# Kernel optimization log

Measured on AMD Instinct MI355X. Metric: run time of the kernel, lower is better.

## Reference

```python
import jax, jax.numpy as jnp
import numpy as np

LAYERS, BLOCKS = 10, 3
N_BLK = LAYERS * BLOCKS
RC, SC, K = 128, 128, 2
IN_CH, COND_CH, OUT_CH = 256, 80, 256
DILATIONS = tuple(2 ** (i % LAYERS) for i in range(N_BLK))
INV_SQRT2 = 0.70710678118


def conv1x1(x, w, b):
    # x: [B, I, T], w: [O, I], b: [O] -> [B, O, T]
    return jnp.einsum('oi,bit->bot', w, x) + b[None, :, None]


def causal_conv(x, w, b, dilation):
    # x: [B, C, T], w: [O, I, K]; left-pad by (K-1)*d == torch pad-both + right slice
    pad = (w.shape[2] - 1) * dilation
    y = jax.lax.conv_general_dilated(
        x, w, window_strides=(1,), padding=[(pad, 0)],
        rhs_dilation=(dilation,), dimension_numbers=('NCH', 'OIH', 'NCH'))
    return y + b[None, :, None]


def setup_inputs() -> dict:
    key = jax.random.key(0)
    ks = jax.random.split(key, 20)
    s = 0.05
    B, T = 2, 8000
    inp = {
        'x': jax.random.normal(ks[0], (B, IN_CH, T), jnp.float32),
        'condition': jax.random.normal(ks[1], (B, COND_CH, T), jnp.float32),
        'input_w': jax.random.normal(ks[2], (RC, IN_CH), jnp.float32) * s,
        'input_b': jax.random.normal(ks[3], (RC,), jnp.float32) * s,
        'dil_w': jax.random.normal(ks[4], (N_BLK, RC, RC, K), jnp.float32) * s,
        'dil_b': jax.random.normal(ks[5], (N_BLK, RC), jnp.float32) * s,
        'gate_w': jax.random.normal(ks[6], (N_BLK, RC, RC), jnp.float32) * s,
        'gate_b': jax.random.normal(ks[7], (N_BLK, RC), jnp.float32) * s,
        'cond_w': jax.random.normal(ks[8], (N_BLK, RC, COND_CH), jnp.float32) * s,
        'cond_b': jax.random.normal(ks[9], (N_BLK, RC), jnp.float32) * s,
        'condg_w': jax.random.normal(ks[10], (N_BLK, RC, COND_CH), jnp.float32) * s,
        'condg_b': jax.random.normal(ks[11], (N_BLK, RC), jnp.float32) * s,
        'res_w': jax.random.normal(ks[12], (N_BLK, RC, RC), jnp.float32) * s,
        'res_b': jax.random.normal(ks[13], (N_BLK, RC), jnp.float32) * s,
        'skip_w': jax.random.normal(ks[14], (N_BLK, SC, RC), jnp.float32) * s,
        'skip_b': jax.random.normal(ks[15], (N_BLK, SC), jnp.float32) * s,
        'out1_w': jax.random.normal(ks[16], (SC, SC), jnp.float32) * s,
        'out1_b': jax.random.normal(ks[17], (SC,), jnp.float32) * s,
        'out2_w': jax.random.normal(ks[18], (OUT_CH, SC), jnp.float32) * s,
        'out2_b': jax.random.normal(ks[19], (OUT_CH,), jnp.float32) * s,
    }
    return inp


def reference(x, condition, input_w, input_b, dil_w, dil_b, gate_w, gate_b,
              cond_w, cond_b, condg_w, condg_b, res_w, res_b,
              skip_w, skip_b, out1_w, out1_b, out2_w, out2_b):
    h = conv1x1(x, input_w, input_b)  # [B, RC, T]
    skip = jnp.zeros_like(conv1x1(h, skip_w[0], skip_b[0]) * 0)  # [B, SC, T]
    for i, d in enumerate(DILATIONS):
        a = causal_conv(h, dil_w[i], dil_b[i], d) + conv1x1(condition, cond_w[i], cond_b[i])
        g = conv1x1(h, gate_w[i], gate_b[i]) + conv1x1(condition, condg_w[i], condg_b[i])
        out = jnp.tanh(a) * jax.nn.sigmoid(g)
        h = (h + conv1x1(out, res_w[i], res_b[i])) * INV_SQRT2
        skip = skip + conv1x1(out, skip_w[i], skip_b[i])
    y = jax.nn.relu(conv1x1(skip, out1_w, out1_b))
    return conv1x1(y, out2_w, out2_b)  # [B, 256, T]
```

## Files before the change

kernel.cpp:

```cpp
#include <hip/hip_runtime.h>

#define T_LEN 8000
#define NTPB 125
#define NBLK 250
#define NLAYER 30
#define GUARD 512
#define HROWS (GUARD + T_LEN)
#define SLAB (HROWS * 128)
#define INV_SQRT2 0.70710678118f

typedef short bf16x8 __attribute__((ext_vector_type(8)));
typedef unsigned uint2v __attribute__((ext_vector_type(2)));
typedef unsigned uint4v __attribute__((ext_vector_type(4)));
typedef float f32x4 __attribute__((ext_vector_type(4)));

#define R_HT  0
#define R_OUT 8192
#define R_CND 16384
#define WB0   22528
#define WB1   38912
#define LDS_SHORTS 55296

#define KLINE 4096
#define LS 106496
#define C1 16384
#define C2 32768
#define C3 49152
#define C4 57344
#define C5 73728
#define C6 90112
#define IN_OFF   3194880
#define OUT1_OFF 3227648
#define OUT2_OFF 3244032

__device__ __forceinline__ unsigned short f2bf_u(float f) {
    union { float f; unsigned u; } v; v.f = f;
    unsigned u = v.u + 0x7FFFu + ((v.u >> 16) & 1u);
    return (unsigned short)(u >> 16);
}
__device__ __forceinline__ short f2bf(float f) { return (short)f2bf_u(f); }

__device__ __forceinline__ unsigned cvtpk(float lo, float hi) {
    unsigned r;
    asm("v_cvt_pk_bf16_f32 %0, %1, %2" : "=v"(r) : "v"(lo), "v"(hi));
    return r;
}

__device__ __forceinline__ float gated_act(float av, float gv) {
    float e  = __expf(-2.f * fabsf(av));
    float th = (1.f - e) * __builtin_amdgcn_rcpf(1.f + e);
    th = (av < 0.f) ? -th : th;
    float sg = __builtin_amdgcn_rcpf(1.f + __expf(-gv));
    return th * sg;
}

__device__ __forceinline__ void ldg16_sc1(bf16x8* d, const short* p) {
    asm volatile("global_load_dwordx4 %0, %1, off sc1" : "=v"(*d) : "v"(p));
}
__device__ __forceinline__ void stg8_sc1(short* p, uint2v v) {
    asm volatile("global_store_dwordx2 %0, %1, off sc1" : : "v"(p), "v"(v) : "memory");
}
__device__ __forceinline__ void st_flag(int* p, int v) {
    __hip_atomic_store(p, v, __ATOMIC_RELAXED, __HIP_MEMORY_SCOPE_AGENT);
}
__device__ __forceinline__ void wait_ge(const int* p, int v) {
    while (__hip_atomic_load(p, __ATOMIC_RELAXED, __HIP_MEMORY_SCOPE_AGENT) < v)
        __builtin_amdgcn_s_sleep(1);
}

__device__ __forceinline__ f32x4 mfma_(bf16x8 a, bf16x8 b, f32x4 c) {
    return __builtin_amdgcn_mfma_f32_16x16x32_bf16(a, b, c, 0, 0, 0);
}

__device__ __forceinline__ void gload_lds16(const short* g, short* l) {
    __builtin_amdgcn_global_load_lds(
        (const __attribute__((address_space(1))) unsigned int*)g,
        (__attribute__((address_space(3))) unsigned int*)l, 16, 0, 0);
}
__device__ __forceinline__ void stageW2(const short* src, short* dst, int wv, int lane) {
    gload_lds16(src + wv * 512 + lane * 8, dst + wv * 512);
    gload_lds16(src + (16 + wv) * 512 + lane * 8, dst + (16 + wv) * 512);
}
__device__ __forceinline__ void stageW1(const short* src, short* dst, int wv, int lane) {
    gload_lds16(src + wv * 512 + lane * 8, dst + wv * 512);
}

template<int NP>
__device__ __forceinline__ void pairN(const short* wb, const short* sm, int boff,
                                      int ks0, int lg, int awoff,
                                      f32x4* ac0, f32x4* ac1)
{
#pragma unroll
    for (int p = 0; p < NP; ++p) {
        bf16x8 B = *(const bf16x8*)&sm[boff + ((ks0 + p) * 4 + lg) * 512];
#pragma unroll
        for (int mt = 0; mt < 2; ++mt) {
            bf16x8 a0 = *(const bf16x8*)&wb[p * 8192 + awoff + mt * 512];
            ac0[mt] = mfma_(a0, B, ac0[mt]);
            bf16x8 a1 = *(const bf16x8*)&wb[p * 8192 + 4096 + awoff + mt * 512];
            ac1[mt] = mfma_(a1, B, ac1[mt]);
        }
    }
}
template<int NP>
__device__ __forceinline__ void singleN(const short* wb, const short* sm, int boff,
                                        int ks0, int lg, int awoff, f32x4* ac)
{
#pragma unroll
    for (int p = 0; p < NP; ++p) {
        bf16x8 B = *(const bf16x8*)&sm[boff + ((ks0 + p) * 4 + lg) * 512];
#pragma unroll
        for (int mt = 0; mt < 2; ++mt) {
            bf16x8 a = *(const bf16x8*)&wb[p * 4096 + awoff + mt * 512];
            ac[mt] = mfma_(a, B, ac[mt]);
        }
    }
}

__global__ __launch_bounds__(256) void k_pack(
    const float* __restrict__ dil_w, const float* __restrict__ gate_w,
    const float* __restrict__ cond_w, const float* __restrict__ condg_w,
    const float* __restrict__ res_w, const float* __restrict__ skip_w,
    const float* __restrict__ input_w, const float* __restrict__ out1_w,
    const float* __restrict__ out2_w,
    const float* __restrict__ dil_b, const float* __restrict__ cond_b,
    const float* __restrict__ gate_b, const float* __restrict__ condg_b,
    short* __restrict__ wp, short* __restrict__ hbt, int* __restrict__ flg)
{
    int gid = blockIdx.x * 256 + threadIdx.x;
    if (gid < 512) flg[gid] = 0;
    {
        int g2 = gid - 512;
        if (g2 >= 0 && g2 < 262144) {
            unsigned* hb32 = (unsigned*)hbt;
            int slab = g2 >> 15, off = g2 & 32767;
            hb32[(size_t)slab * (SLAB / 2) + off] = 0u;
        }
    }
    if (gid >= 6400 * 64) return;
    int fid = gid >> 6, lane = gid & 63;
    int lr = lane & 15, lg = lane >> 4;
    float v[8];
    if (fid < 6240) {
        int layer = fid / 208;
        int r = fid - layer * 208;
        int kl = r >> 3, f = r & 7;
        int m = f * 16 + lr;
        size_t mi = (size_t)layer * 128 + m;
        int mat, ks;
        if      (kl < 8)  { mat = (kl & 1) ? 2 : 1; ks = kl >> 1; }
        else if (kl < 14) { mat = (kl & 1) ? 4 : 3; ks = (kl - 8) >> 1; }
        else if (kl < 18) { mat = 0; ks = kl - 14; }
        else              { mat = (kl & 1) ? 6 : 5; ks = (kl - 18) >> 1; }
        int kb = ks * 32 + lg * 8;
#pragma unroll
        for (int e = 0; e < 8; ++e) {
            int k = kb + e;
            float val;
            switch (mat) {
                case 0:  val = dil_w[(mi * 128 + k) * 2];     break;
                case 1:  val = dil_w[(mi * 128 + k) * 2 + 1]; break;
                case 2:  val = gate_w[mi * 128 + k]; break;
                case 3:  val = (k < 80) ? cond_w[mi * 80 + k]
                               : ((k == 80) ? dil_b[mi] + cond_b[mi] : 0.f); break;
                case 4:  val = (k < 80) ? condg_w[mi * 80 + k]
                               : ((k == 80) ? gate_b[mi] + condg_b[mi] : 0.f); break;
                case 5:  val = res_w[mi * 128 + k]; break;
                default: val = skip_w[mi * 128 + k]; break;
            }
            v[e] = val;
        }
    } else if (fid < 6304) {
        int f = fid - 6240; int ks = f >> 3, fr = f & 7;
        int m = fr * 16 + lr; int kb = ks * 32 + lg * 8;
#pragma unroll
        for (int e = 0; e < 8; ++e) v[e] = input_w[(size_t)m * 256 + kb + e];
    } else if (fid < 6336) {
        int f = fid - 6304; int ks = f >> 3, fr = f & 7;
        int m = fr * 16 + lr; int kb = ks * 32 + lg * 8;
#pragma unroll
        for (int e = 0; e < 8; ++e) v[e] = out1_w[(size_t)m * 128 + kb + e];
    } else {
        int f = fid - 6336; int mt = f & 15; int ks = f >> 4;
        int m = mt * 16 + lr; int kb = ks * 32 + lg * 8;
#pragma unroll
        for (int e = 0; e < 8; ++e) v[e] = out2_w[(size_t)m * 128 + kb + e];
    }
    short* dst = wp + (size_t)fid * 512 + lane * 8;
#pragma unroll
    for (int e = 0; e < 8; ++e) dst[e] = f2bf(v[e]);
}

__global__ __launch_bounds__(1024, 4) void k_wavenet(
    const float* __restrict__ x, const float* __restrict__ cond,
    const short* __restrict__ wp, short* __restrict__ hbt,
    const float* __restrict__ ib, const float* __restrict__ rbias,
    const float* __restrict__ sbias, const float* __restrict__ b1,
    const float* __restrict__ b2, float* __restrict__ outp,
    int* __restrict__ rdy, int* __restrict__ dn)
{
    __shared__ __align__(16) short sm[LDS_SHORTS];

    const int tid  = threadIdx.x;
    const int lane = tid & 63;
    const int wv   = __builtin_amdgcn_readfirstlane(tid >> 6);
    const int wm   = wv & 3;
    const int wn   = wv >> 2;
    const int lr   = lane & 15, lg = lane >> 4;
    const int bidx = blockIdx.x;
    const int b    = bidx / NTPB;
    const int ti   = bidx - b * NTPB;
    const int t0   = ti * 64;
    const int tl   = wn * 16 + lr;
    const int tg   = t0 + tl;
    const int tl8  = tl * 8;
    const int lane8 = lane * 8;
    const int awoff = wm * 1024 + lane8;
    const int chA  = wm * 32 + lg * 4;
    const int kbA  = wm * 4 + (lg >> 1);
    const int e0   = (lg & 1) * 4;

    stageW2(wp + IN_OFF, (short*)&sm[WB0], wv, lane);
    stageW2(wp + IN_OFF + 16384, (short*)&sm[WB1], wv, lane);
    {
        const float* xb = x + (size_t)b * 256 * T_LEN + t0 + lane;
#pragma unroll
        for (int it = 0; it < 2; ++it) {
            int kb = wv * 2 + it;
            unsigned pk[4];
#pragma unroll
            for (int e = 0; e < 4; ++e)
                pk[e] = cvtpk(xb[(size_t)(kb * 8 + 2 * e) * T_LEN],
                              xb[(size_t)(kb * 8 + 2 * e + 1) * T_LEN]);
            *(uint4v*)&sm[(kb * 64 + lane) * 8] = *(uint4v*)pk;
        }
        if (wv < 12) {
            const float* cb = cond + (size_t)b * 80 * T_LEN + t0 + lane;
            unsigned pk[4];
#pragma unroll
            for (int e = 0; e < 4; ++e) {
                int c0 = wv * 8 + 2 * e, c1 = c0 + 1;
                float v0 = (c0 < 80) ? cb[(size_t)c0 * T_LEN] : ((c0 == 80) ? 1.f : 0.f);
                float v1 = (c1 < 80) ? cb[(size_t)c1 * T_LEN] : 0.f;
                pk[e] = cvtpk(v0, v1);
            }
            *(uint4v*)&sm[R_CND + (wv * 64 + lane) * 8] = *(uint4v*)pk;
        }
    }
    __syncthreads();

    f32x4 hres[2] = {{0.f,0.f,0.f,0.f},{0.f,0.f,0.f,0.f}};
    {
        f32x4 acc[2] = {{0.f,0.f,0.f,0.f},{0.f,0.f,0.f,0.f}};
        singleN<4>((const short*)&sm[WB0], sm, tl8, 0, lg, awoff, acc);
        singleN<4>((const short*)&sm[WB1], sm, tl8, 4, lg, awoff, acc);
#pragma unroll
        for (int mt = 0; mt < 2; ++mt) {
            int cb0 = chA + mt * 16;
            f32x4 bv = {ib[cb0], ib[cb0 + 1], ib[cb0 + 2], ib[cb0 + 3]};
            hres[mt] = acc[mt] + bv;
        }
    }
    __syncthreads();
    {
        short* hrow = hbt + (size_t)b * SLAB + (size_t)(GUARD + tg) * 128 + chA;
#pragma unroll
        for (int mt = 0; mt < 2; ++mt) {
            uint2v hv = {cvtpk(hres[mt][0], hres[mt][1]), cvtpk(hres[mt][2], hres[mt][3])};
            stg8_sc1(hrow + mt * 16, hv);
            *(uint2v*)&sm[R_HT + ((kbA + mt * 2) * 64 + tl) * 8 + e0] = hv;
        }
    }
    __syncthreads();
    if (tid == 0) st_flag(&rdy[bidx], 1);

    f32x4 skp[2] = {{0.f,0.f,0.f,0.f},{0.f,0.f,0.f,0.f}};

    for (int li = 0; li < NLAYER; ++li) {
        const int d   = 1 << (li % 10);
        const int ksh = (d + 63) >> 6;
        const short* wl  = wp + (size_t)li * LS;
        const short* hcb = hbt + (size_t)((li & 3) * 2 + b) * SLAB;
        short*       hnb = hbt + (size_t)(((li + 1) & 3) * 2 + b) * SLAB;

        stageW2(wl, (short*)&sm[WB0], wv, lane);
        __syncthreads();
        if (lane == 0 && ti >= ksh) wait_ge(&rdy[bidx - ksh], li + 1);
        bf16x8 Bg[4];
        {
            const short* hr = hcb + (size_t)(GUARD + tg - d) * 128 + lg * 8;
#pragma unroll
            for (int ks = 0; ks < 4; ++ks) ldg16_sc1(&Bg[ks], hr + ks * 32);
        }
        stageW2(wl + C1, (short*)&sm[WB1], wv, lane);
        f32x4 aa[2] = {{0.f,0.f,0.f,0.f},{0.f,0.f,0.f,0.f}};
        f32x4 ag[2] = {{0.f,0.f,0.f,0.f},{0.f,0.f,0.f,0.f}};
        pairN<2>((const short*)&sm[WB0], sm, R_HT + tl8, 0, lg, awoff, aa, ag);
        __syncthreads();
        if (tid == 0) st_flag(&dn[bidx], li + 1);
        stageW2(wl + C2, (short*)&sm[WB0], wv, lane);
        pairN<2>((const short*)&sm[WB1], sm, R_HT + tl8, 2, lg, awoff, aa, ag);
        __syncthreads();
        stageW1(wl + C3, (short*)&sm[WB1], wv, lane);
        pairN<2>((const short*)&sm[WB0], sm, R_CND + tl8, 0, lg, awoff, aa, ag);
        __syncthreads();
        stageW2(wl + C4, (short*)&sm[WB0], wv, lane);
        pairN<1>((const short*)&sm[WB1], sm, R_CND + tl8, 2, lg, awoff, aa, ag);
        __syncthreads();
        stageW2(wl + C5, (short*)&sm[WB1], wv, lane);
        {
            const short* wb = (const short*)&sm[WB0];
#pragma unroll
            for (int ks = 0; ks < 4; ++ks) {
#pragma unroll
                for (int mt = 0; mt < 2; ++mt) {
                    bf16x8 a = *(const bf16x8*)&wb[ks * 4096 + awoff + mt * 512];
                    aa[mt] = mfma_(a, Bg[ks], aa[mt]);
                }
            }
        }
#pragma unroll
        for (int mt = 0; mt < 2; ++mt) {
            uint2v ov = {cvtpk(gated_act(aa[mt][0], ag[mt][0]), gated_act(aa[mt][1], ag[mt][1])),
                         cvtpk(gated_act(aa[mt][2], ag[mt][2]), gated_act(aa[mt][3], ag[mt][3]))};
            *(uint2v*)&sm[R_OUT + ((kbA + mt * 2) * 64 + tl) * 8 + e0] = ov;
        }
        __syncthreads();
        stageW2(wl + C6, (short*)&sm[WB0], wv, lane);
        f32x4 ar[2]  = {{0.f,0.f,0.f,0.f},{0.f,0.f,0.f,0.f}};
        f32x4 as2[2] = {{0.f,0.f,0.f,0.f},{0.f,0.f,0.f,0.f}};
        pairN<2>((const short*)&sm[WB1], sm, R_OUT + tl8, 0, lg, awoff, ar, as2);
        __syncthreads();
        pairN<2>((const short*)&sm[WB0], sm, R_OUT + tl8, 2, lg, awoff, ar, as2);

        const float* rbl = rbias + li * 128 + chA;
        const float* sbl = sbias + li * 128 + chA;
#pragma unroll
        for (int mt = 0; mt < 2; ++mt) {
            f32x4 rbv = {rbl[mt*16], rbl[mt*16+1], rbl[mt*16+2], rbl[mt*16+3]};
            f32x4 sbv = {sbl[mt*16], sbl[mt*16+1], sbl[mt*16+2], sbl[mt*16+3]};
            skp[mt]  = skp[mt] + as2[mt] + sbv;
            hres[mt] = (hres[mt] + ar[mt] + rbv) * INV_SQRT2;
        }
        if (li < NLAYER - 1) {
            if (lane == 0 && li >= 3) {
                int d3 = 1 << ((li - 3) % 10);
                int k3 = (d3 + 63) >> 6;
                if (ti + k3 < NTPB) wait_ge(&dn[bidx + k3], li - 2);
            }
            short* hrow = hnb + (size_t)(GUARD + tg) * 128 + chA;
#pragma unroll
            for (int mt = 0; mt < 2; ++mt) {
                uint2v hv = {cvtpk(hres[mt][0], hres[mt][1]), cvtpk(hres[mt][2], hres[mt][3])};
                stg8_sc1(hrow + mt * 16, hv);
                *(uint2v*)&sm[R_HT + ((kbA + mt * 2) * 64 + tl) * 8 + e0] = hv;
            }
        }
        __syncthreads();
        if (tid == 0 && li < NLAYER - 1) st_flag(&rdy[bidx], li + 2);
    }

#pragma unroll
    for (int mt = 0; mt < 2; ++mt) {
        uint2v sv = {cvtpk(skp[mt][0], skp[mt][1]), cvtpk(skp[mt][2], skp[mt][3])};
        *(uint2v*)&sm[R_HT + ((kbA + mt * 2) * 64 + tl) * 8 + e0] = sv;
    }
    stageW2(wp + OUT1_OFF, (short*)&sm[WB0], wv, lane);
    stageW2(wp + OUT2_OFF, (short*)&sm[WB1], wv, lane);
    __syncthreads();
    f32x4 ay[2] = {{0.f,0.f,0.f,0.f},{0.f,0.f,0.f,0.f}};
    singleN<4>((const short*)&sm[WB0], sm, R_HT + tl8, 0, lg, awoff, ay);
#pragma unroll
    for (int mt = 0; mt < 2; ++mt) {
        int cb0 = chA + mt * 16;
        float y0 = fmaxf(ay[mt][0] + b1[cb0],     0.f);
        float y1 = fmaxf(ay[mt][1] + b1[cb0 + 1], 0.f);
        float y2 = fmaxf(ay[mt][2] + b1[cb0 + 2], 0.f);
        float y3 = fmaxf(ay[mt][3] + b1[cb0 + 3], 0.f);
        uint2v yv = {cvtpk(y0, y1), cvtpk(y2, y3)};
        *(uint2v*)&sm[R_OUT + ((kbA + mt * 2) * 64 + tl) * 8 + e0] = yv;
    }
    __syncthreads();
    stageW2(wp + OUT2_OFF + 16384, (short*)&sm[WB0], wv, lane);
    f32x4 ao[4] = {{0.f,0.f,0.f,0.f},{0.f,0.f,0.f,0.f},
                   {0.f,0.f,0.f,0.f},{0.f,0.f,0.f,0.f}};
    {
        const short* wb = (const short*)&sm[WB1];
#pragma unroll
        for (int ksp = 0; ksp < 2; ++ksp) {
            bf16x8 B = *(const bf16x8*)&sm[R_OUT + tl8 + (ksp * 4 + lg) * 512];
#pragma unroll
            for (int mt = 0; mt < 4; ++mt) {
                int fg = 4 * wm + mt;
                bf16x8 A = *(const bf16x8*)&wb[(ksp * 2 + (fg >> 3)) * 4096 + (fg & 7) * 512 + lane8];
                ao[mt] = mfma_(A, B, ao[mt]);
            }
        }
    }
    __syncthreads();
    {
        const short* wb = (const short*)&sm[WB0];
#pragma unroll
        for (int ksp = 0; ksp < 2; ++ksp) {
            bf16x8 B = *(const bf16x8*)&sm[R_OUT + tl8 + ((2 + ksp) * 4 + lg) * 512];
#pragma unroll
            for (int mt = 0; mt < 4; ++mt) {
                int fg = 4 * wm + mt;
                bf16x8 A = *(const bf16x8*)&wb[(ksp * 2 + (fg >> 3)) * 4096 + (fg & 7) * 512 + lane8];
                ao[mt] = mfma_(A, B, ao[mt]);
            }
        }
    }
#pragma unroll
    for (int mt = 0; mt < 4; ++mt) {
        int ch2 = wm * 64 + mt * 16 + lg * 4;
        float* op = outp + ((size_t)(b * 256 + ch2)) * T_LEN + tg;
        op[0]         = ao[mt][0] + b2[ch2];
        op[T_LEN]     = ao[mt][1] + b2[ch2 + 1];
        op[2 * T_LEN] = ao[mt][2] + b2[ch2 + 2];
        op[3 * T_LEN] = ao[mt][3] + b2[ch2 + 3];
    }
}

extern "C" void kernel_launch(void* const* d_in, const int* in_sizes, int n_in,
                              void* d_out, int out_size, void* d_ws, size_t ws_size,
                              hipStream_t stream)
{
    const float* x       = (const float*)d_in[0];
    const float* cond    = (const float*)d_in[1];
    const float* input_w = (const float*)d_in[2];
    const float* input_b = (const float*)d_in[3];
    const float* dil_w   = (const float*)d_in[4];
    const float* dil_b   = (const float*)d_in[5];
    const float* gate_w  = (const float*)d_in[6];
    const float* gate_b  = (const float*)d_in[7];
    const float* cond_w  = (const float*)d_in[8];
    const float* cond_b  = (const float*)d_in[9];
    const float* condg_w = (const float*)d_in[10];
    const float* condg_b = (const float*)d_in[11];
    const float* res_w   = (const float*)d_in[12];
    const float* res_b   = (const float*)d_in[13];
    const float* skip_w  = (const float*)d_in[14];
    const float* skip_b  = (const float*)d_in[15];
    const float* out1_w  = (const float*)d_in[16];
    const float* out1_b  = (const float*)d_in[17];
    const float* out2_w  = (const float*)d_in[18];
    const float* out2_b  = (const float*)d_in[19];
    float* outp = (float*)d_out;

    short* wpk = (short*)d_ws;
    short* hbt = wpk + (size_t)6400 * 512;
    int*   flg = (int*)(hbt + (size_t)8 * SLAB);
    int*   rdy = flg;
    int*   dn  = flg + 256;

    k_pack<<<1600, 256, 0, stream>>>(dil_w, gate_w, cond_w, condg_w, res_w, skip_w,
                                     input_w, out1_w, out2_w,
                                     dil_b, cond_b, gate_b, condg_b, wpk, hbt, flg);

    void* args[] = {(void*)&x, (void*)&cond, (void*)&wpk, (void*)&hbt,
                    (void*)&input_b, (void*)&res_b, (void*)&skip_b,
                    (void*)&out1_b, (void*)&out2_b, (void*)&outp,
                    (void*)&rdy, (void*)&dn};
    hipLaunchCooperativeKernel((void*)k_wavenet, dim3(NBLK), dim3(1024), args, 0, stream);
}
```

Before: 289.5 us.

## Triple-buffer per-layer weight staging with vmcnt waits instead of full barriers

Replaces the two LDS weight buffers with three rotating buffers, so each layer issues up to three chunk loads ahead and waits only with targeted s_waitcnt vmcnt counts plus raw s_barrier rather than __syncthreads. Bias loads are hoisted to the start of the layer, and the neighbour 'done' flag wait is moved earlier, overlapping the final residual/skip MFMA chunk. The epilogue stages all output weights up front and drops one barrier. The intent is to hide global-to-LDS weight latency behind the MFMA work. In exchange it uses more LDS, and correctness now rests on hand-counted vmcnt values matching how stageW1 and stageW2 issue their loads.

```diff
diff --git a/kernel.cpp b/kernel.cpp
--- a/kernel.cpp
+++ b/kernel.cpp
@@ -17,9 +17,8 @@
 #define R_HT  0
 #define R_OUT 8192
 #define R_CND 16384
-#define WB0   22528
-#define WB1   38912
-#define LDS_SHORTS 55296
+#define WBASE 22528
+#define LDS_SHORTS 71680
 
 #define KLINE 4096
 #define LS 106496
@@ -32,6 +31,10 @@
 #define IN_OFF   3194880
 #define OUT1_OFF 3227648
 #define OUT2_OFF 3244032
+
+#define WAITV(N) asm volatile("s_waitcnt vmcnt(" #N ")" ::: "memory")
+#define LGKM0    asm volatile("s_waitcnt lgkmcnt(0)" ::: "memory")
+#define BAR      asm volatile("s_barrier" ::: "memory")
 
 __device__ __forceinline__ unsigned short f2bf_u(float f) {
     union { float f; unsigned u; } v; v.f = f;
@@ -220,8 +223,8 @@
     const int kbA  = wm * 4 + (lg >> 1);
     const int e0   = (lg & 1) * 4;
 
-    stageW2(wp + IN_OFF, (short*)&sm[WB0], wv, lane);
-    stageW2(wp + IN_OFF + 16384, (short*)&sm[WB1], wv, lane);
+    stageW2(wp + IN_OFF, (short*)&sm[WBASE], wv, lane);
+    stageW2(wp + IN_OFF + 16384, (short*)&sm[WBASE + 16384], wv, lane);
     {
         const float* xb = x + (size_t)b * 256 * T_LEN + t0 + lane;
 #pragma unroll
@@ -252,8 +255,8 @@
     f32x4 hres[2] = {{0.f,0.f,0.f,0.f},{0.f,0.f,0.f,0.f}};
     {
         f32x4 acc[2] = {{0.f,0.f,0.f,0.f},{0.f,0.f,0.f,0.f}};
-        singleN<4>((const short*)&sm[WB0], sm, tl8, 0, lg, awoff, acc);
-        singleN<4>((const short*)&sm[WB1], sm, tl8, 4, lg, awoff, acc);
+        singleN<4>((const short*)&sm[WBASE], sm, tl8, 0, lg, awoff, acc);
+        singleN<4>((const short*)&sm[WBASE + 16384], sm, tl8, 4, lg, awoff, acc);
 #pragma unroll
         for (int mt = 0; mt < 2; ++mt) {
             int cb0 = chA + mt * 16;
@@ -271,50 +274,75 @@
             *(uint2v*)&sm[R_HT + ((kbA + mt * 2) * 64 + tl) * 8 + e0] = hv;
         }
     }
+    asm volatile("s_waitcnt vmcnt(0)" ::: "memory");
     __syncthreads();
     if (tid == 0) st_flag(&rdy[bidx], 1);
 
     f32x4 skp[2] = {{0.f,0.f,0.f,0.f},{0.f,0.f,0.f,0.f}};
 
+    int rot = 0;
     for (int li = 0; li < NLAYER; ++li) {
         const int d   = 1 << (li % 10);
         const int ksh = (d + 63) >> 6;
         const short* wl  = wp + (size_t)li * LS;
         const short* hcb = hbt + (size_t)((li & 3) * 2 + b) * SLAB;
         short*       hnb = hbt + (size_t)(((li + 1) & 3) * 2 + b) * SLAB;
-
-        stageW2(wl, (short*)&sm[WB0], wv, lane);
-        __syncthreads();
+        const int rA = rot;
+        const int rB = (rot + 1) % 3;
+        const int rC = (rot + 2) % 3;
+        short* const sA = (short*)&sm[WBASE + rA * 16384];
+        short* const sB = (short*)&sm[WBASE + rB * 16384];
+        short* const sC = (short*)&sm[WBASE + rC * 16384];
+
         if (lane == 0 && ti >= ksh) wait_ge(&rdy[bidx - ksh], li + 1);
+
+        f32x4 rbv[2], sbv[2];
+        {
+            const float* rbl = rbias + li * 128 + chA;
+            const float* sbl = sbias + li * 128 + chA;
+#pragma unroll
+            for (int mt = 0; mt < 2; ++mt) {
+                rbv[mt] = (f32x4){rbl[mt*16], rbl[mt*16+1], rbl[mt*16+2], rbl[mt*16+3]};
+                sbv[mt] = (f32x4){sbl[mt*16], sbl[mt*16+1], sbl[mt*16+2], sbl[mt*16+3]};
+            }
+        }
+
+        stageW2(wl, sA, wv, lane);
         bf16x8 Bg[4];
         {
             const short* hr = hcb + (size_t)(GUARD + tg - d) * 128 + lg * 8;
 #pragma unroll
             for (int ks = 0; ks < 4; ++ks) ldg16_sc1(&Bg[ks], hr + ks * 32);
         }
-        stageW2(wl + C1, (short*)&sm[WB1], wv, lane);
+        stageW2(wl + C1, sB, wv, lane);
+        stageW2(wl + C2, sC, wv, lane);
+
+        WAITV(8); BAR;
         f32x4 aa[2] = {{0.f,0.f,0.f,0.f},{0.f,0.f,0.f,0.f}};
         f32x4 ag[2] = {{0.f,0.f,0.f,0.f},{0.f,0.f,0.f,0.f}};
-        pairN<2>((const short*)&sm[WB0], sm, R_HT + tl8, 0, lg, awoff, aa, ag);
-        __syncthreads();
+        pairN<2>(sA, sm, R_HT + tl8, 0, lg, awoff, aa, ag);
+
+        WAITV(2); BAR;
         if (tid == 0) st_flag(&dn[bidx], li + 1);
-        stageW2(wl + C2, (short*)&sm[WB0], wv, lane);
-        pairN<2>((const short*)&sm[WB1], sm, R_HT + tl8, 2, lg, awoff, aa, ag);
-        __syncthreads();
-        stageW1(wl + C3, (short*)&sm[WB1], wv, lane);
-        pairN<2>((const short*)&sm[WB0], sm, R_CND + tl8, 0, lg, awoff, aa, ag);
-        __syncthreads();
-        stageW2(wl + C4, (short*)&sm[WB0], wv, lane);
-        pairN<1>((const short*)&sm[WB1], sm, R_CND + tl8, 2, lg, awoff, aa, ag);
-        __syncthreads();
-        stageW2(wl + C5, (short*)&sm[WB1], wv, lane);
+        stageW1(wl + C3, sA, wv, lane);
+        pairN<2>(sB, sm, R_HT + tl8, 2, lg, awoff, aa, ag);
+
+        WAITV(1); BAR;
+        stageW2(wl + C4, sB, wv, lane);
+        pairN<2>(sC, sm, R_CND + tl8, 0, lg, awoff, aa, ag);
+
+        WAITV(2); BAR;
+        stageW2(wl + C5, sC, wv, lane);
+        pairN<1>(sA, sm, R_CND + tl8, 2, lg, awoff, aa, ag);
+
+        WAITV(2); BAR;
+        stageW2(wl + C6, sA, wv, lane);
         {
-            const short* wb = (const short*)&sm[WB0];
 #pragma unroll
             for (int ks = 0; ks < 4; ++ks) {
 #pragma unroll
                 for (int mt = 0; mt < 2; ++mt) {
-                    bf16x8 a = *(const bf16x8*)&wb[ks * 4096 + awoff + mt * 512];
+                    bf16x8 a = *(const bf16x8*)&sB[ks * 4096 + awoff + mt * 512];
                     aa[mt] = mfma_(a, Bg[ks], aa[mt]);
                 }
             }
@@ -325,29 +353,25 @@
                          cvtpk(gated_act(aa[mt][2], ag[mt][2]), gated_act(aa[mt][3], ag[mt][3]))};
             *(uint2v*)&sm[R_OUT + ((kbA + mt * 2) * 64 + tl) * 8 + e0] = ov;
         }
-        __syncthreads();
-        stageW2(wl + C6, (short*)&sm[WB0], wv, lane);
+        WAITV(2); LGKM0; BAR;
+
         f32x4 ar[2]  = {{0.f,0.f,0.f,0.f},{0.f,0.f,0.f,0.f}};
         f32x4 as2[2] = {{0.f,0.f,0.f,0.f},{0.f,0.f,0.f,0.f}};
-        pairN<2>((const short*)&sm[WB1], sm, R_OUT + tl8, 0, lg, awoff, ar, as2);
-        __syncthreads();
-        pairN<2>((const short*)&sm[WB0], sm, R_OUT + tl8, 2, lg, awoff, ar, as2);
-
-        const float* rbl = rbias + li * 128 + chA;
-        const float* sbl = sbias + li * 128 + chA;
-#pragma unroll
-        for (int mt = 0; mt < 2; ++mt) {
-            f32x4 rbv = {rbl[mt*16], rbl[mt*16+1], rbl[mt*16+2], rbl[mt*16+3]};
-            f32x4 sbv = {sbl[mt*16], sbl[mt*16+1], sbl[mt*16+2], sbl[mt*16+3]};
-            skp[mt]  = skp[mt] + as2[mt] + sbv;
-            hres[mt] = (hres[mt] + ar[mt] + rbv) * INV_SQRT2;
+        pairN<2>(sC, sm, R_OUT + tl8, 0, lg, awoff, ar, as2);
+        if (lane == 0 && li >= 3) {
+            int d3 = 1 << ((li - 3) % 10);
+            int k3 = (d3 + 63) >> 6;
+            if (ti + k3 < NTPB) wait_ge(&dn[bidx + k3], li - 2);
+        }
+        WAITV(0); BAR;
+        pairN<2>(sA, sm, R_OUT + tl8, 2, lg, awoff, ar, as2);
+
+#pragma unroll
+        for (int mt = 0; mt < 2; ++mt) {
+            skp[mt]  = skp[mt] + as2[mt] + sbv[mt];
+            hres[mt] = (hres[mt] + ar[mt] + rbv[mt]) * INV_SQRT2;
         }
         if (li < NLAYER - 1) {
-            if (lane == 0 && li >= 3) {
-                int d3 = 1 << ((li - 3) % 10);
-                int k3 = (d3 + 63) >> 6;
-                if (ti + k3 < NTPB) wait_ge(&dn[bidx + k3], li - 2);
-            }
             short* hrow = hnb + (size_t)(GUARD + tg) * 128 + chA;
 #pragma unroll
             for (int mt = 0; mt < 2; ++mt) {
@@ -356,20 +380,22 @@
                 *(uint2v*)&sm[R_HT + ((kbA + mt * 2) * 64 + tl) * 8 + e0] = hv;
             }
         }
-        __syncthreads();
+        WAITV(0); LGKM0; BAR;
         if (tid == 0 && li < NLAYER - 1) st_flag(&rdy[bidx], li + 2);
-    }
-
+        rot = (rot + 1) % 3;
+    }
+
+    stageW2(wp + OUT1_OFF, (short*)&sm[WBASE], wv, lane);
+    stageW2(wp + OUT2_OFF, (short*)&sm[WBASE + 16384], wv, lane);
+    stageW2(wp + OUT2_OFF + 16384, (short*)&sm[WBASE + 32768], wv, lane);
 #pragma unroll
     for (int mt = 0; mt < 2; ++mt) {
         uint2v sv = {cvtpk(skp[mt][0], skp[mt][1]), cvtpk(skp[mt][2], skp[mt][3])};
         *(uint2v*)&sm[R_HT + ((kbA + mt * 2) * 64 + tl) * 8 + e0] = sv;
     }
-    stageW2(wp + OUT1_OFF, (short*)&sm[WB0], wv, lane);
-    stageW2(wp + OUT2_OFF, (short*)&sm[WB1], wv, lane);
     __syncthreads();
     f32x4 ay[2] = {{0.f,0.f,0.f,0.f},{0.f,0.f,0.f,0.f}};
-    singleN<4>((const short*)&sm[WB0], sm, R_HT + tl8, 0, lg, awoff, ay);
+    singleN<4>((const short*)&sm[WBASE], sm, R_HT + tl8, 0, lg, awoff, ay);
 #pragma unroll
     for (int mt = 0; mt < 2; ++mt) {
         int cb0 = chA + mt * 16;
@@ -381,32 +407,28 @@
         *(uint2v*)&sm[R_OUT + ((kbA + mt * 2) * 64 + tl) * 8 + e0] = yv;
     }
     __syncthreads();
-    stageW2(wp + OUT2_OFF + 16384, (short*)&sm[WB0], wv, lane);
     f32x4 ao[4] = {{0.f,0.f,0.f,0.f},{0.f,0.f,0.f,0.f},
                    {0.f,0.f,0.f,0.f},{0.f,0.f,0.f,0.f}};
     {
-        const short* wb = (const short*)&sm[WB1];
+        const short* w2a = (const short*)&sm[WBASE + 16384];
+        const short* w2b = (const short*)&sm[WBASE + 32768];
 #pragma unroll
         for (int ksp = 0; ksp < 2; ++ksp) {
             bf16x8 B = *(const bf16x8*)&sm[R_OUT + tl8 + (ksp * 4 + lg) * 512];
 #pragma unroll
             for (int mt = 0; mt < 4; ++mt) {
                 int fg = 4 * wm + mt;
-                bf16x8 A = *(const bf16x8*)&wb[(ksp * 2 + (fg >> 3)) * 4096 + (fg & 7) * 512 + lane8];
+                bf16x8 A = *(const bf16x8*)&w2a[(ksp * 2 + (fg >> 3)) * 4096 + (fg & 7) * 512 + lane8];
                 ao[mt] = mfma_(A, B, ao[mt]);
             }
         }
-    }
-    __syncthreads();
-    {
-        const short* wb = (const short*)&sm[WB0];
 #pragma unroll
         for (int ksp = 0; ksp < 2; ++ksp) {
             bf16x8 B = *(const bf16x8*)&sm[R_OUT + tl8 + ((2 + ksp) * 4 + lg) * 512];
 #pragma unroll
             for (int mt = 0; mt < 4; ++mt) {
                 int fg = 4 * wm + mt;
-                bf16x8 A = *(const bf16x8*)&wb[(ksp * 2 + (fg >> 3)) * 4096 + (fg & 7) * 512 + lane8];
+                bf16x8 A = *(const bf16x8*)&w2b[(ksp * 2 + (fg >> 3)) * 4096 + (fg & 7) * 512 + lane8];
                 ao[mt] = mfma_(A, B, ao[mt]);
             }
         }
@@ -462,5 +484,5 @@
                     (void*)&input_b, (void*)&res_b, (void*)&skip_b,
                     (void*)&out1_b, (void*)&out2_b, (void*)&outp,
                     (void*)&rdy, (void*)&dn};
-    hipLaunchCooperativeKernel((void*)k_wavenet, dim3(NBLK), dim3(1024), args, 0, stream);
-}
+    (void)hipLaunchCooperativeKernel((void*)k_wavenet, dim3(NBLK), dim3(1024), args, 0, stream);
+}
```

New measurement: 328.4 us. +13.5%, slower.

## Halve block to 8 waves, each wave computing two time tiles

Applied to the files above, without the earlier changes.

Shrinks the workgroup from 16 to 8 waves, so each wave now covers two 16-column time tiles. Every weight A-fragment read from LDS feeds two MFMAs instead of one, which roughly halves LDS weight traffic per MFMA. Weight staging is rewritten so 8 waves load the same tiles, and the final output GEMM is re-tiled accordingly. The cost is more accumulator registers per wave and fewer waves per block to hide latency. An explicit vmcnt wait is added before the ready flag is published.

```diff
diff --git a/kernel.cpp b/kernel.cpp
--- a/kernel.cpp
+++ b/kernel.cpp
@@ -17,11 +17,9 @@
 #define R_HT  0
 #define R_OUT 8192
 #define R_CND 16384
-#define WB0   22528
-#define WB1   38912
+#define WBASE 22528
 #define LDS_SHORTS 55296
 
-#define KLINE 4096
 #define LS 106496
 #define C1 16384
 #define C2 32768
@@ -45,7 +43,6 @@
     asm("v_cvt_pk_bf16_f32 %0, %1, %2" : "=v"(r) : "v"(lo), "v"(hi));
     return r;
 }
-
 __device__ __forceinline__ float gated_act(float av, float gv) {
     float e  = __expf(-2.f * fabsf(av));
     float th = (1.f - e) * __builtin_amdgcn_rcpf(1.f + e);
@@ -53,7 +50,6 @@
     float sg = __builtin_amdgcn_rcpf(1.f + __expf(-gv));
     return th * sg;
 }
-
 __device__ __forceinline__ void ldg16_sc1(bf16x8* d, const short* p) {
     asm volatile("global_load_dwordx4 %0, %1, off sc1" : "=v"(*d) : "v"(p));
 }
@@ -67,52 +63,65 @@
     while (__hip_atomic_load(p, __ATOMIC_RELAXED, __HIP_MEMORY_SCOPE_AGENT) < v)
         __builtin_amdgcn_s_sleep(1);
 }
-
 __device__ __forceinline__ f32x4 mfma_(bf16x8 a, bf16x8 b, f32x4 c) {
     return __builtin_amdgcn_mfma_f32_16x16x32_bf16(a, b, c, 0, 0, 0);
 }
-
 __device__ __forceinline__ void gload_lds16(const short* g, short* l) {
     __builtin_amdgcn_global_load_lds(
         (const __attribute__((address_space(1))) unsigned int*)g,
         (__attribute__((address_space(3))) unsigned int*)l, 16, 0, 0);
 }
-__device__ __forceinline__ void stageW2(const short* src, short* dst, int wv, int lane) {
-    gload_lds16(src + wv * 512 + lane * 8, dst + wv * 512);
-    gload_lds16(src + (16 + wv) * 512 + lane * 8, dst + (16 + wv) * 512);
-}
-__device__ __forceinline__ void stageW1(const short* src, short* dst, int wv, int lane) {
-    gload_lds16(src + wv * 512 + lane * 8, dst + wv * 512);
+__device__ __forceinline__ void stage32(const short* src, short* dst, int wv, int lane) {
+#pragma unroll
+    for (int r = 0; r < 4; ++r) {
+        int s = (r * 8 + wv) * 512;
+        gload_lds16(src + s + lane * 8, dst + s);
+    }
+}
+__device__ __forceinline__ void stage16(const short* src, short* dst, int wv, int lane) {
+#pragma unroll
+    for (int r = 0; r < 2; ++r) {
+        int s = (r * 8 + wv) * 512;
+        gload_lds16(src + s + lane * 8, dst + s);
+    }
 }
 
 template<int NP>
-__device__ __forceinline__ void pairN(const short* wb, const short* sm, int boff,
-                                      int ks0, int lg, int awoff,
-                                      f32x4* ac0, f32x4* ac1)
+__device__ __forceinline__ void pairT2(const short* wb, const short* smp, int reg,
+                                       int ks0, int tc0, int tc1, int lg, int awoff,
+                                       f32x4 (&A)[2][2], f32x4 (&G)[2][2])
 {
 #pragma unroll
     for (int p = 0; p < NP; ++p) {
-        bf16x8 B = *(const bf16x8*)&sm[boff + ((ks0 + p) * 4 + lg) * 512];
+        int slot = reg + ((ks0 + p) * 4 + lg) * 512;
+        bf16x8 B0 = *(const bf16x8*)&smp[slot + tc0 * 8];
+        bf16x8 B1 = *(const bf16x8*)&smp[slot + tc1 * 8];
 #pragma unroll
         for (int mt = 0; mt < 2; ++mt) {
             bf16x8 a0 = *(const bf16x8*)&wb[p * 8192 + awoff + mt * 512];
-            ac0[mt] = mfma_(a0, B, ac0[mt]);
+            A[mt][0] = mfma_(a0, B0, A[mt][0]);
+            A[mt][1] = mfma_(a0, B1, A[mt][1]);
             bf16x8 a1 = *(const bf16x8*)&wb[p * 8192 + 4096 + awoff + mt * 512];
-            ac1[mt] = mfma_(a1, B, ac1[mt]);
+            G[mt][0] = mfma_(a1, B0, G[mt][0]);
+            G[mt][1] = mfma_(a1, B1, G[mt][1]);
         }
     }
 }
 template<int NP>
-__device__ __forceinline__ void singleN(const short* wb, const short* sm, int boff,
-                                        int ks0, int lg, int awoff, f32x4* ac)
+__device__ __forceinline__ void singleT2(const short* wb, const short* smp, int reg,
+                                         int ks0, int tc0, int tc1, int lg, int awoff,
+                                         f32x4 (&ac)[2][2])
 {
 #pragma unroll
     for (int p = 0; p < NP; ++p) {
-        bf16x8 B = *(const bf16x8*)&sm[boff + ((ks0 + p) * 4 + lg) * 512];
+        int slot = reg + ((ks0 + p) * 4 + lg) * 512;
+        bf16x8 B0 = *(const bf16x8*)&smp[slot + tc0 * 8];
+        bf16x8 B1 = *(const bf16x8*)&smp[slot + tc1 * 8];
 #pragma unroll
         for (int mt = 0; mt < 2; ++mt) {
             bf16x8 a = *(const bf16x8*)&wb[p * 4096 + awoff + mt * 512];
-            ac[mt] = mfma_(a, B, ac[mt]);
+            ac[mt][0] = mfma_(a, B0, ac[mt][0]);
+            ac[mt][1] = mfma_(a, B1, ac[mt][1]);
         }
     }
 }
@@ -191,7 +200,7 @@
     for (int e = 0; e < 8; ++e) dst[e] = f2bf(v[e]);
 }
 
-__global__ __launch_bounds__(1024, 4) void k_wavenet(
+__global__ __launch_bounds__(512, 2) void k_wavenet(
     const float* __restrict__ x, const float* __restrict__ cond,
     const short* __restrict__ wp, short* __restrict__ hbt,
     const float* __restrict__ ib, const float* __restrict__ rbias,
@@ -205,28 +214,32 @@
     const int lane = tid & 63;
     const int wv   = __builtin_amdgcn_readfirstlane(tid >> 6);
     const int wm   = wv & 3;
-    const int wn   = wv >> 2;
+    const int wt   = wv >> 2;
     const int lr   = lane & 15, lg = lane >> 4;
     const int bidx = blockIdx.x;
     const int b    = bidx / NTPB;
     const int ti   = bidx - b * NTPB;
     const int t0   = ti * 64;
-    const int tl   = wn * 16 + lr;
-    const int tg   = t0 + tl;
-    const int tl8  = tl * 8;
+    const int tc0  = wt * 32 + lr;
+    const int tc1  = tc0 + 16;
+    const int tg0  = t0 + tc0;
+    const int tg1  = t0 + tc1;
     const int lane8 = lane * 8;
     const int awoff = wm * 1024 + lane8;
     const int chA  = wm * 32 + lg * 4;
     const int kbA  = wm * 4 + (lg >> 1);
     const int e0   = (lg & 1) * 4;
 
-    stageW2(wp + IN_OFF, (short*)&sm[WB0], wv, lane);
-    stageW2(wp + IN_OFF + 16384, (short*)&sm[WB1], wv, lane);
+    short* const W0 = (short*)&sm[WBASE];
+    short* const W1 = (short*)&sm[WBASE + 16384];
+
+    stage32(wp + IN_OFF, W0, wv, lane);
+    stage32(wp + IN_OFF + 16384, W1, wv, lane);
     {
         const float* xb = x + (size_t)b * 256 * T_LEN + t0 + lane;
 #pragma unroll
-        for (int it = 0; it < 2; ++it) {
-            int kb = wv * 2 + it;
+        for (int it = 0; it < 4; ++it) {
+            int kb = wv * 4 + it;
             unsigned pk[4];
 #pragma unroll
             for (int e = 0; e < 4; ++e)
@@ -234,47 +247,55 @@
                               xb[(size_t)(kb * 8 + 2 * e + 1) * T_LEN]);
             *(uint4v*)&sm[(kb * 64 + lane) * 8] = *(uint4v*)pk;
         }
-        if (wv < 12) {
+        if (wv < 6) {
             const float* cb = cond + (size_t)b * 80 * T_LEN + t0 + lane;
-            unsigned pk[4];
-#pragma unroll
-            for (int e = 0; e < 4; ++e) {
-                int c0 = wv * 8 + 2 * e, c1 = c0 + 1;
-                float v0 = (c0 < 80) ? cb[(size_t)c0 * T_LEN] : ((c0 == 80) ? 1.f : 0.f);
-                float v1 = (c1 < 80) ? cb[(size_t)c1 * T_LEN] : 0.f;
-                pk[e] = cvtpk(v0, v1);
+#pragma unroll
+            for (int it = 0; it < 2; ++it) {
+                int kb = wv * 2 + it;
+                unsigned pk[4];
+#pragma unroll
+                for (int e = 0; e < 4; ++e) {
+                    int c0 = kb * 8 + 2 * e, c1 = c0 + 1;
+                    float v0 = (c0 < 80) ? cb[(size_t)c0 * T_LEN] : ((c0 == 80) ? 1.f : 0.f);
+                    float v1 = (c1 < 80) ? cb[(size_t)c1 * T_LEN] : 0.f;
+                    pk[e] = cvtpk(v0, v1);
+                }
+                *(uint4v*)&sm[R_CND + (kb * 64 + lane) * 8] = *(uint4v*)pk;
             }
-            *(uint4v*)&sm[R_CND + (wv * 64 + lane) * 8] = *(uint4v*)pk;
         }
     }
     __syncthreads();
 
-    f32x4 hres[2] = {{0.f,0.f,0.f,0.f},{0.f,0.f,0.f,0.f}};
+    f32x4 hres[2][2], skp[2][2];
     {
-        f32x4 acc[2] = {{0.f,0.f,0.f,0.f},{0.f,0.f,0.f,0.f}};
-        singleN<4>((const short*)&sm[WB0], sm, tl8, 0, lg, awoff, acc);
-        singleN<4>((const short*)&sm[WB1], sm, tl8, 4, lg, awoff, acc);
+        f32x4 acc[2][2] = {{{0,0,0,0},{0,0,0,0}},{{0,0,0,0},{0,0,0,0}}};
+        singleT2<4>(W0, sm, 0, 0, tc0, tc1, lg, awoff, acc);
+        singleT2<4>(W1, sm, 0, 4, tc0, tc1, lg, awoff, acc);
+        __syncthreads();
 #pragma unroll
         for (int mt = 0; mt < 2; ++mt) {
             int cb0 = chA + mt * 16;
             f32x4 bv = {ib[cb0], ib[cb0 + 1], ib[cb0 + 2], ib[cb0 + 3]};
-            hres[mt] = acc[mt] + bv;
-        }
-    }
-    __syncthreads();
-    {
-        short* hrow = hbt + (size_t)b * SLAB + (size_t)(GUARD + tg) * 128 + chA;
-#pragma unroll
-        for (int mt = 0; mt < 2; ++mt) {
-            uint2v hv = {cvtpk(hres[mt][0], hres[mt][1]), cvtpk(hres[mt][2], hres[mt][3])};
-            stg8_sc1(hrow + mt * 16, hv);
-            *(uint2v*)&sm[R_HT + ((kbA + mt * 2) * 64 + tl) * 8 + e0] = hv;
-        }
-    }
+            hres[mt][0] = acc[mt][0] + bv;
+            hres[mt][1] = acc[mt][1] + bv;
+            skp[mt][0] = (f32x4){0.f,0.f,0.f,0.f};
+            skp[mt][1] = (f32x4){0.f,0.f,0.f,0.f};
+        }
+        short* hr0 = hbt + (size_t)b * SLAB + (size_t)(GUARD + tg0) * 128 + chA;
+        short* hr1 = hbt + (size_t)b * SLAB + (size_t)(GUARD + tg1) * 128 + chA;
+#pragma unroll
+        for (int mt = 0; mt < 2; ++mt) {
+            uint2v h0 = {cvtpk(hres[mt][0][0], hres[mt][0][1]), cvtpk(hres[mt][0][2], hres[mt][0][3])};
+            uint2v h1 = {cvtpk(hres[mt][1][0], hres[mt][1][1]), cvtpk(hres[mt][1][2], hres[mt][1][3])};
+            stg8_sc1(hr0 + mt * 16, h0);
+            stg8_sc1(hr1 + mt * 16, h1);
+            *(uint2v*)&sm[R_HT + ((kbA + mt * 2) * 64 + tc0) * 8 + e0] = h0;
+            *(uint2v*)&sm[R_HT + ((kbA + mt * 2) * 64 + tc1) * 8 + e0] = h1;
+        }
+    }
+    asm volatile("s_waitcnt vmcnt(0)" ::: "memory");
     __syncthreads();
     if (tid == 0) st_flag(&rdy[bidx], 1);
-
-    f32x4 skp[2] = {{0.f,0.f,0.f,0.f},{0.f,0.f,0.f,0.f}};
 
     for (int li = 0; li < NLAYER; ++li) {
         const int d   = 1 << (li % 10);
@@ -283,55 +304,66 @@
         const short* hcb = hbt + (size_t)((li & 3) * 2 + b) * SLAB;
         short*       hnb = hbt + (size_t)(((li + 1) & 3) * 2 + b) * SLAB;
 
-        stageW2(wl, (short*)&sm[WB0], wv, lane);
+        stage32(wl, W0, wv, lane);
         __syncthreads();
         if (lane == 0 && ti >= ksh) wait_ge(&rdy[bidx - ksh], li + 1);
-        bf16x8 Bg[4];
+        bf16x8 Bg[2][4];
         {
-            const short* hr = hcb + (size_t)(GUARD + tg - d) * 128 + lg * 8;
-#pragma unroll
-            for (int ks = 0; ks < 4; ++ks) ldg16_sc1(&Bg[ks], hr + ks * 32);
-        }
-        stageW2(wl + C1, (short*)&sm[WB1], wv, lane);
-        f32x4 aa[2] = {{0.f,0.f,0.f,0.f},{0.f,0.f,0.f,0.f}};
-        f32x4 ag[2] = {{0.f,0.f,0.f,0.f},{0.f,0.f,0.f,0.f}};
-        pairN<2>((const short*)&sm[WB0], sm, R_HT + tl8, 0, lg, awoff, aa, ag);
+            const short* hr0 = hcb + (size_t)(GUARD + tg0 - d) * 128 + lg * 8;
+            const short* hr1 = hcb + (size_t)(GUARD + tg1 - d) * 128 + lg * 8;
+#pragma unroll
+            for (int ks = 0; ks < 4; ++ks) {
+                ldg16_sc1(&Bg[0][ks], hr0 + ks * 32);
+                ldg16_sc1(&Bg[1][ks], hr1 + ks * 32);
+            }
+        }
+        stage32(wl + C1, W1, wv, lane);
+        f32x4 aa[2][2] = {{{0,0,0,0},{0,0,0,0}},{{0,0,0,0},{0,0,0,0}}};
+        f32x4 ag[2][2] = {{{0,0,0,0},{0,0,0,0}},{{0,0,0,0},{0,0,0,0}}};
+        pairT2<2>(W0, sm, R_HT, 0, tc0, tc1, lg, awoff, aa, ag);
         __syncthreads();
         if (tid == 0) st_flag(&dn[bidx], li + 1);
-        stageW2(wl + C2, (short*)&sm[WB0], wv, lane);
-        pairN<2>((const short*)&sm[WB1], sm, R_HT + tl8, 2, lg, awoff, aa, ag);
-        __syncthreads();
-        stageW1(wl + C3, (short*)&sm[WB1], wv, lane);
-        pairN<2>((const short*)&sm[WB0], sm, R_CND + tl8, 0, lg, awoff, aa, ag);
-        __syncthreads();
-        stageW2(wl + C4, (short*)&sm[WB0], wv, lane);
-        pairN<1>((const short*)&sm[WB1], sm, R_CND + tl8, 2, lg, awoff, aa, ag);
-        __syncthreads();
-        stageW2(wl + C5, (short*)&sm[WB1], wv, lane);
+        stage32(wl + C2, W0, wv, lane);
+        pairT2<2>(W1, sm, R_HT, 2, tc0, tc1, lg, awoff, aa, ag);
+        __syncthreads();
+        stage16(wl + C3, W1, wv, lane);
+        pairT2<2>(W0, sm, R_CND, 0, tc0, tc1, lg, awoff, aa, ag);
+        __syncthreads();
+        stage32(wl + C4, W0, wv, lane);
+        pairT2<1>(W1, sm, R_CND, 2, tc0, tc1, lg, awoff, aa, ag);
+        __syncthreads();
+        stage32(wl + C5, W1, wv, lane);
         {
-            const short* wb = (const short*)&sm[WB0];
 #pragma unroll
             for (int ks = 0; ks < 4; ++ks) {
 #pragma unroll
                 for (int mt = 0; mt < 2; ++mt) {
-                    bf16x8 a = *(const bf16x8*)&wb[ks * 4096 + awoff + mt * 512];
-                    aa[mt] = mfma_(a, Bg[ks], aa[mt]);
+                    bf16x8 a = *(const bf16x8*)&W0[ks * 4096 + awoff + mt * 512];
+                    aa[mt][0] = mfma_(a, Bg[0][ks], aa[mt][0]);
+                    aa[mt][1] = mfma_(a, Bg[1][ks], aa[mt][1]);
                 }
             }
         }
 #pragma unroll
         for (int mt = 0; mt < 2; ++mt) {
-            uint2v ov = {cvtpk(gated_act(aa[mt][0], ag[mt][0]), gated_act(aa[mt][1], ag[mt][1])),
-                         cvtpk(gated_act(aa[mt][2], ag[mt][2]), gated_act(aa[mt][3], ag[mt][3]))};
-            *(uint2v*)&sm[R_OUT + ((kbA + mt * 2) * 64 + tl) * 8 + e0] = ov;
-        }
-        __syncthreads();
-        stageW2(wl + C6, (short*)&sm[WB0], wv, lane);
-        f32x4 ar[2]  = {{0.f,0.f,0.f,0.f},{0.f,0.f,0.f,0.f}};
-        f32x4 as2[2] = {{0.f,0.f,0.f,0.f},{0.f,0.f,0.f,0.f}};
-        pairN<2>((const short*)&sm[WB1], sm, R_OUT + tl8, 0, lg, awoff, ar, as2);
-        __syncthreads();
-        pairN<2>((const short*)&sm[WB0], sm, R_OUT + tl8, 2, lg, awoff, ar, as2);
+            uint2v o0 = {cvtpk(gated_act(aa[mt][0][0], ag[mt][0][0]),
+                               gated_act(aa[mt][0][1], ag[mt][0][1])),
+                         cvtpk(gated_act(aa[mt][0][2], ag[mt][0][2]),
+                               gated_act(aa[mt][0][3], ag[mt][0][3]))};
+            uint2v o1 = {cvtpk(gated_act(aa[mt][1][0], ag[mt][1][0]),
+                               gated_act(aa[mt][1][1], ag[mt][1][1])),
+                         cvtpk(gated_act(aa[mt][1][2], ag[mt][1][2]),
+                               gated_act(aa[mt][1][3], ag[mt][1][3]))};
+            *(uint2v*)&sm[R_OUT + ((kbA + mt * 2) * 64 + tc0) * 8 + e0] = o0;
+            *(uint2v*)&sm[R_OUT + ((kbA + mt * 2) * 64 + tc1) * 8 + e0] = o1;
+        }
+        __syncthreads();
+        stage32(wl + C6, W0, wv, lane);
+        f32x4 ar[2][2]  = {{{0,0,0,0},{0,0,0,0}},{{0,0,0,0},{0,0,0,0}}};
+        f32x4 as2[2][2] = {{{0,0,0,0},{0,0,0,0}},{{0,0,0,0},{0,0,0,0}}};
+        pairT2<2>(W1, sm, R_OUT, 0, tc0, tc1, lg, awoff, ar, as2);
+        __syncthreads();
+        pairT2<2>(W0, sm, R_OUT, 2, tc0, tc1, lg, awoff, ar, as2);
 
         const float* rbl = rbias + li * 128 + chA;
         const float* sbl = sbias + li * 128 + chA;
@@ -339,8 +371,10 @@
         for (int mt = 0; mt < 2; ++mt) {
             f32x4 rbv = {rbl[mt*16], rbl[mt*16+1], rbl[mt*16+2], rbl[mt*16+3]};
             f32x4 sbv = {sbl[mt*16], sbl[mt*16+1], sbl[mt*16+2], sbl[mt*16+3]};
-            skp[mt]  = skp[mt] + as2[mt] + sbv;
-            hres[mt] = (hres[mt] + ar[mt] + rbv) * INV_SQRT2;
+            hres[mt][0] = (hres[mt][0] + ar[mt][0] + rbv) * INV_SQRT2;
+            hres[mt][1] = (hres[mt][1] + ar[mt][1] + rbv) * INV_SQRT2;
+            skp[mt][0]  = skp[mt][0] + as2[mt][0] + sbv;
+            skp[mt][1]  = skp[mt][1] + as2[mt][1] + sbv;
         }
         if (li < NLAYER - 1) {
             if (lane == 0 && li >= 3) {
@@ -348,12 +382,16 @@
                 int k3 = (d3 + 63) >> 6;
                 if (ti + k3 < NTPB) wait_ge(&dn[bidx + k3], li - 2);
             }
-            short* hrow = hnb + (size_t)(GUARD + tg) * 128 + chA;
+            short* hr0 = hnb + (size_t)(GUARD + tg0) * 128 + chA;
+            short* hr1 = hnb + (size_t)(GUARD + tg1) * 128 + chA;
 #pragma unroll
             for (int mt = 0; mt < 2; ++mt) {
-                uint2v hv = {cvtpk(hres[mt][0], hres[mt][1]), cvtpk(hres[mt][2], hres[mt][3])};
-                stg8_sc1(hrow + mt * 16, hv);
-                *(uint2v*)&sm[R_HT + ((kbA + mt * 2) * 64 + tl) * 8 + e0] = hv;
+                uint2v h0 = {cvtpk(hres[mt][0][0], hres[mt][0][1]), cvtpk(hres[mt][0][2], hres[mt][0][3])};
+                uint2v h1 = {cvtpk(hres[mt][1][0], hres[mt][1][1]), cvtpk(hres[mt][1][2], hres[mt][1][3])};
+                stg8_sc1(hr0 + mt * 16, h0);
+                stg8_sc1(hr1 + mt * 16, h1);
+                *(uint2v*)&sm[R_HT + ((kbA + mt * 2) * 64 + tc0) * 8 + e0] = h0;
+                *(uint2v*)&sm[R_HT + ((kbA + mt * 2) * 64 + tc1) * 8 + e0] = h1;
             }
         }
         __syncthreads();
@@ -362,63 +400,60 @@
 
 #pragma unroll
     for (int mt = 0; mt < 2; ++mt) {
-        uint2v sv = {cvtpk(skp[mt][0], skp[mt][1]), cvtpk(skp[mt][2], skp[mt][3])};
-        *(uint2v*)&sm[R_HT + ((kbA + mt * 2) * 64 + tl) * 8 + e0] = sv;
-    }
-    stageW2(wp + OUT1_OFF, (short*)&sm[WB0], wv, lane);
-    stageW2(wp + OUT2_OFF, (short*)&sm[WB1], wv, lane);
+        uint2v s0 = {cvtpk(skp[mt][0][0], skp[mt][0][1]), cvtpk(skp[mt][0][2], skp[mt][0][3])};
+        uint2v s1 = {cvtpk(skp[mt][1][0], skp[mt][1][1]), cvtpk(skp[mt][1][2], skp[mt][1][3])};
+        *(uint2v*)&sm[R_HT + ((kbA + mt * 2) * 64 + tc0) * 8 + e0] = s0;
+        *(uint2v*)&sm[R_HT + ((kbA + mt * 2) * 64 + tc1) * 8 + e0] = s1;
+    }
+    stage32(wp + OUT1_OFF, W0, wv, lane);
+    stage32(wp + OUT2_OFF, W1, wv, lane);
     __syncthreads();
-    f32x4 ay[2] = {{0.f,0.f,0.f,0.f},{0.f,0.f,0.f,0.f}};
-    singleN<4>((const short*)&sm[WB0], sm, R_HT + tl8, 0, lg, awoff, ay);
+    f32x4 ay[2][2] = {{{0,0,0,0},{0,0,0,0}},{{0,0,0,0},{0,0,0,0}}};
+    singleT2<4>(W0, sm, R_HT, 0, tc0, tc1, lg, awoff, ay);
+    __syncthreads();
+    stage32(wp + OUT2_OFF + 16384, W0, wv, lane);
 #pragma unroll
     for (int mt = 0; mt < 2; ++mt) {
         int cb0 = chA + mt * 16;
-        float y0 = fmaxf(ay[mt][0] + b1[cb0],     0.f);
-        float y1 = fmaxf(ay[mt][1] + b1[cb0 + 1], 0.f);
-        float y2 = fmaxf(ay[mt][2] + b1[cb0 + 2], 0.f);
-        float y3 = fmaxf(ay[mt][3] + b1[cb0 + 3], 0.f);
-        uint2v yv = {cvtpk(y0, y1), cvtpk(y2, y3)};
-        *(uint2v*)&sm[R_OUT + ((kbA + mt * 2) * 64 + tl) * 8 + e0] = yv;
+        f32x4 bv = {b1[cb0], b1[cb0+1], b1[cb0+2], b1[cb0+3]};
+        f32x4 y0 = ay[mt][0] + bv, y1 = ay[mt][1] + bv;
+        uint2v p0 = {cvtpk(fmaxf(y0[0],0.f), fmaxf(y0[1],0.f)),
+                     cvtpk(fmaxf(y0[2],0.f), fmaxf(y0[3],0.f))};
+        uint2v p1 = {cvtpk(fmaxf(y1[0],0.f), fmaxf(y1[1],0.f)),
+                     cvtpk(fmaxf(y1[2],0.f), fmaxf(y1[3],0.f))};
+        *(uint2v*)&sm[R_OUT + ((kbA + mt * 2) * 64 + tc0) * 8 + e0] = p0;
+        *(uint2v*)&sm[R_OUT + ((kbA + mt * 2) * 64 + tc1) * 8 + e0] = p1;
     }
     __syncthreads();
-    stageW2(wp + OUT2_OFF + 16384, (short*)&sm[WB0], wv, lane);
-    f32x4 ao[4] = {{0.f,0.f,0.f,0.f},{0.f,0.f,0.f,0.f},
-                   {0.f,0.f,0.f,0.f},{0.f,0.f,0.f,0.f}};
-    {
-        const short* wb = (const short*)&sm[WB1];
-#pragma unroll
-        for (int ksp = 0; ksp < 2; ++ksp) {
-            bf16x8 B = *(const bf16x8*)&sm[R_OUT + tl8 + (ksp * 4 + lg) * 512];
-#pragma unroll
-            for (int mt = 0; mt < 4; ++mt) {
-                int fg = 4 * wm + mt;
-                bf16x8 A = *(const bf16x8*)&wb[(ksp * 2 + (fg >> 3)) * 4096 + (fg & 7) * 512 + lane8];
-                ao[mt] = mfma_(A, B, ao[mt]);
-            }
-        }
-    }
-    __syncthreads();
-    {
-        const short* wb = (const short*)&sm[WB0];
-#pragma unroll
-        for (int ksp = 0; ksp < 2; ++ksp) {
-            bf16x8 B = *(const bf16x8*)&sm[R_OUT + tl8 + ((2 + ksp) * 4 + lg) * 512];
-#pragma unroll
-            for (int mt = 0; mt < 4; ++mt) {
-                int fg = 4 * wm + mt;
-                bf16x8 A = *(const bf16x8*)&wb[(ksp * 2 + (fg >> 3)) * 4096 + (fg & 7) * 512 + lane8];
-                ao[mt] = mfma_(A, B, ao[mt]);
-            }
-        }
-    }
-#pragma unroll
-    for (int mt = 0; mt < 4; ++mt) {
-        int ch2 = wm * 64 + mt * 16 + lg * 4;
-        float* op = outp + ((size_t)(b * 256 + ch2)) * T_LEN + tg;
-        op[0]         = ao[mt][0] + b2[ch2];
-        op[T_LEN]     = ao[mt][1] + b2[ch2 + 1];
-        op[2 * T_LEN] = ao[mt][2] + b2[ch2 + 2];
-        op[3 * T_LEN] = ao[mt][3] + b2[ch2 + 3];
+    f32x4 ao[2][4] = {{{0,0,0,0},{0,0,0,0},{0,0,0,0},{0,0,0,0}},
+                      {{0,0,0,0},{0,0,0,0},{0,0,0,0},{0,0,0,0}}};
+#pragma unroll
+    for (int ks = 0; ks < 4; ++ks) {
+        const short* wch = (ks < 2) ? W1 : W0;
+        int kk = ks & 1;
+        bf16x8 Bf[4];
+#pragma unroll
+        for (int tf = 0; tf < 4; ++tf)
+            Bf[tf] = *(const bf16x8*)&sm[R_OUT + (ks * 4 + lg) * 512 + (tf * 16 + lr) * 8];
+#pragma unroll
+        for (int mt = 0; mt < 2; ++mt) {
+            bf16x8 A = *(const bf16x8*)&wch[((kk * 16) + wv * 2 + mt) * 512 + lane8];
+#pragma unroll
+            for (int tf = 0; tf < 4; ++tf)
+                ao[mt][tf] = mfma_(A, Bf[tf], ao[mt][tf]);
+        }
+    }
+#pragma unroll
+    for (int mt = 0; mt < 2; ++mt) {
+        int ch2 = (wv * 2 + mt) * 16 + lg * 4;
+#pragma unroll
+        for (int tf = 0; tf < 4; ++tf) {
+            float* op = outp + ((size_t)(b * 256 + ch2)) * T_LEN + t0 + tf * 16 + lr;
+            op[0]         = ao[mt][tf][0] + b2[ch2];
+            op[T_LEN]     = ao[mt][tf][1] + b2[ch2 + 1];
+            op[2 * T_LEN] = ao[mt][tf][2] + b2[ch2 + 2];
+            op[3 * T_LEN] = ao[mt][tf][3] + b2[ch2 + 3];
+        }
     }
 }
 
@@ -462,5 +497,5 @@
                     (void*)&input_b, (void*)&res_b, (void*)&skip_b,
                     (void*)&out1_b, (void*)&out2_b, (void*)&outp,
                     (void*)&rdy, (void*)&dn};
-    hipLaunchCooperativeKernel((void*)k_wavenet, dim3(NBLK), dim3(1024), args, 0, stream);
-}
+    (void)hipLaunchCooperativeKernel((void*)k_wavenet, dim3(NBLK), dim3(512), args, 0, stream);
+}
```

Measured after the change: 302.5 us. 4.5% more time.
